# Kernel tuning notes

Hardware: AMD Instinct MI355X
Metric: run time of the kernel (lower is better)

## Reference

```python
import math
import jax
import jax.numpy as jnp
import numpy as np
from jax import lax

NH = 256       # n_hidden
KS = 5         # kernel_size
STRIDE = 2
DEPTH_VARIANT = True
B = 64
T = 4096


def _conv1d(x, w, b, stride):
    # x: [B, Cin, L], w: [Cout, Cin, K], torch-style symmetric padding (K-1)//2
    p = (w.shape[2] - 1) // 2
    y = lax.conv_general_dilated(x, w, window_strides=(stride,),
                                 padding=[(p, p)],
                                 dimension_numbers=('NCH', 'OIH', 'NCH'))
    return y + b[None, :, None]


def _seq_mask(x, N):
    m = jnp.arange(x.shape[2])[None, :] < N[:, None]
    return x * m[:, None, :].astype(x.dtype)


def setup_inputs() -> dict:
    key = jax.random.key(0)
    k1, k2, k3, k4, k5, k6 = jax.random.split(key, 6)
    h = jax.random.normal(k1, (B, NH, T), dtype=jnp.float32)
    N = jax.random.randint(k2, (B,), 1, T + 1, dtype=jnp.int32)
    cin1 = NH + (1 if DEPTH_VARIANT else 0)
    s1 = 1.0 / math.sqrt(cin1 * KS)
    s2 = 1.0 / math.sqrt(NH * KS)
    w1 = jax.random.uniform(k3, (2 * NH, cin1, KS), jnp.float32, -s1, s1)
    b1 = jax.random.uniform(k4, (2 * NH,), jnp.float32, -s1, s1)
    w2 = jax.random.uniform(k5, (NH, NH, KS), jnp.float32, -s2, s2)
    b2 = jax.random.uniform(k6, (NH,), jnp.float32, -s2, s2)
    return {"h": h, "N": N, "w1": w1, "b1": b1, "w2": w2, "b2": b2}


def reference(h, N, w1, b1, w2, b2):
    # Faithful to torch Reduce.forward (eval mode, dropout=0).
    # Instead of dynamically pruning finished rows, run all rows for the full
    # (statically known) number of reductions and capture h[:, :, 0] at the
    # depth where each row's N first drops to <= 1. The original output order
    # (grouped by finishing depth, original order within a group) is recovered
    # by a stable argsort on finish depth.
    nh = NH
    batch = h.shape[0]
    captured = jnp.zeros((batch, nh), h.dtype)
    finish_depth = jnp.zeros((batch,), jnp.int32)
    done = jnp.zeros((batch,), bool)
    depth = 0
    while True:
        if DEPTH_VARIANT:
            d = jnp.full((batch, 1, h.shape[2]), math.log1p(depth), h.dtype)
            hh = jnp.concatenate([h, d], axis=1)
        else:
            hh = h
        hh = _seq_mask(hh, N)
        lr = _conv1d(hh, w1, b1, STRIDE)
        N = (N - 1) // STRIDE + 1  # floor((N-1)/stride) + 1
        l = lr[:, :nh]
        r = jax.nn.relu(lr[:, nh:])
        r = _seq_mask(r, N)
        r = _conv1d(r, w2, b2, 1)
        h = jax.nn.relu(l + r)
        newly = (~done) & (N <= 1)
        captured = jnp.where(newly[:, None], h[:, :, 0], captured)
        finish_depth = jnp.where(newly, depth, finish_depth)
        done = done | newly
        depth += 1
        if h.shape[2] <= 1:  # static time length; N <= L so all rows are done
            break
    order = jnp.argsort(finish_depth, stable=True)
    return captured[order]
```

## Files before the change

kernel.cpp:

```cpp
#include <hip/hip_runtime.h>
#include <cmath>
#include <cstdint>


typedef __attribute__((ext_vector_type(8))) __bf16 bf16x8;
typedef __attribute__((ext_vector_type(4))) float f32x4;

union U16B { uint4 u; bf16x8 b; };
__device__ __forceinline__ bf16x8 as_bf16x8(uint4 u) { U16B x; x.u = u; return x.b; }

__device__ __forceinline__ unsigned short bf_hi_bits(float x) {
    union { __bf16 b; unsigned short s; } u; u.b = (__bf16)x; return u.s;
}
__device__ __forceinline__ float bf_hi_f(float x) { return (float)(__bf16)x; }

#define MFMA(a, b, c) __builtin_amdgcn_mfma_f32_16x16x32_bf16(a, b, c, 0, 0, 0)

__global__ void setup_kernel(const int* __restrict__ N0, int* __restrict__ rankfd) {
    __shared__ int fd_s[64];
    int b = threadIdx.x;
    int n = N0[b];
    int d = 0;
    while ((1 << (d + 1)) < n) ++d;
    fd_s[b] = d;
    __syncthreads();
    int myfd = fd_s[b];
    int r = 0;
    for (int i = 0; i < 64; ++i) {
        int f = fd_s[i];
        r += (f < myfd || (f == myfd && i < b)) ? 1 : 0;
    }
    rankfd[b] = r;
    rankfd[64 + b] = myfd;
}

__global__ void prepack_kernel(const float* __restrict__ w1, const float* __restrict__ w2,
                               unsigned short* __restrict__ Whi1, unsigned short* __restrict__ Wlo1,
                               unsigned short* __restrict__ Whi2, unsigned short* __restrict__ Wlo2,
                               float* __restrict__ wd1, float* __restrict__ wsum1) {
    const int T1 = 40 * 32 * 512;
    const int T2 = 40 * 16 * 512;
    int id = blockIdx.x * 256 + threadIdx.x;
    if (id < T1) {
        int chunk = id >> 14;
        int rem = id & 16383;
        int ot = rem >> 9;
        int rem2 = rem & 511;
        int l = rem2 >> 3, j = rem2 & 7;
        int k = chunk >> 3, cc = chunk & 7;
        int oc = ot * 16 + (l & 15);
        int c = cc * 32 + (l >> 4) * 8 + j;
        float wv = w1[oc * 1285 + c * 5 + k];
        Whi1[id] = bf_hi_bits(wv);
        Wlo1[id] = bf_hi_bits(wv - bf_hi_f(wv));
    } else if (id < T1 + T2) {
        int base = id - T1;
        int chunk = base >> 13;
        int rem = base & 8191;
        int ot = rem >> 9;
        int rem2 = rem & 511;
        int l = rem2 >> 3, j = rem2 & 7;
        int k = chunk >> 3, cc = chunk & 7;
        int oc = ot * 16 + (l & 15);
        int c = cc * 32 + (l >> 4) * 8 + j;
        float wv = w2[oc * 1280 + c * 5 + k];
        Whi2[base] = bf_hi_bits(wv);
        Wlo2[base] = bf_hi_bits(wv - bf_hi_f(wv));
    } else if (id < T1 + T2 + 512) {
        int oc = id - T1 - T2;
        float s = 0.f;
        for (int k = 0; k < 5; ++k) {
            float wv = w1[oc * 1285 + 1280 + k];
            wd1[oc * 5 + k] = wv;
            s += wv;
        }
        wsum1[oc] = s;
    }
}

__global__ __launch_bounds__(256, 4)
void transpose_kernel(const float* __restrict__ h, const int* __restrict__ N0,
                      char* __restrict__ H) {
    __shared__ unsigned short sm[2 * 64 * 140];
    const int tid = threadIdx.x;
    const int b = blockIdx.z;
    const int c0 = blockIdx.y * 64;
    const int t0 = blockIdx.x * 128;
    const int n0 = N0[b];
    const int lane32 = tid & 31;
    for (int it = 0; it < 8; ++it) {
        int cl = (tid >> 5) * 8 + it;
        const float* src = h + ((size_t)(b * 256 + c0 + cl)) * 4096 + t0 + lane32 * 4;
        float4 v = *(const float4*)src;
        int gt = t0 + lane32 * 4;
        float f[4] = {v.x, v.y, v.z, v.w};
        ushort4 hi, lo;
        unsigned short* hp = &hi.x;
        unsigned short* lp = &lo.x;
#pragma unroll
        for (int e = 0; e < 4; ++e) {
            float x = (gt + e < n0) ? f[e] : 0.f;
            float xh = bf_hi_f(x);
            hp[e] = bf_hi_bits(x);
            lp[e] = bf_hi_bits(x - xh);
        }
        *(ushort4*)(&sm[cl * 140 + lane32 * 4]) = hi;
        *(ushort4*)(&sm[8960 + cl * 140 + lane32 * 4]) = lo;
    }
    __syncthreads();
    const int sub = tid & 7;
    const int rowp = tid >> 3;
    for (int rep = 0; rep < 8; ++rep) {
        int idx = rowp + 32 * rep;
        int tl = idx >> 1;
        int plane = idx & 1;
        union { unsigned short s[8]; uint4 u; } pk;
#pragma unroll
        for (int j = 0; j < 8; ++j)
            pk.s[j] = sm[plane * 8960 + (sub * 8 + j) * 140 + tl];
        char* dst = H + ((size_t)(b * 4096) + t0 + tl) * 1024 + plane * 512 + c0 * 2 + sub * 16;
        *(uint4*)dst = pk.u;
    }
}

__global__ __launch_bounds__(256, 4)
void conv1_kernel(const char* __restrict__ Hin,
                  const unsigned short* __restrict__ Whi, const unsigned short* __restrict__ Wlo,
                  const float* __restrict__ b1, const float* __restrict__ wd1,
                  const float* __restrict__ wsum1, const int* __restrict__ N0,
                  float* __restrict__ Lout, char* __restrict__ Rout,
                  int T_in, int T_out, int depth, float logd) {
    __shared__ __align__(16) char smem[132 * 256];
    const int tid = threadIdx.x;
    const int w = tid >> 6, l = tid & 63;
    const int b = blockIdx.z;
    const int x_eff = (int)((blockIdx.x + 5u * (blockIdx.z >> 2)) & (gridDim.x - 1));
    const int t0 = x_eff * 64;
    const int n0 = N0[b];
    const int Nb = (n0 + (1 << depth) - 1) >> depth;
    const int Nn = (Nb + 1) >> 1;

    if (t0 >= Nn) {
        if (blockIdx.y == 1) {
            int row = t0 + (tid >> 2);
            if (row < T_out) {
                char* rp = Rout + ((size_t)(b * T_out) + row) * 1024 + (tid & 3) * 256;
                uint4 z = make_uint4(0, 0, 0, 0);
#pragma unroll
                for (int qq = 0; qq < 16; ++qq) *(uint4*)(rp + qq * 16) = z;
            }
        }
        return;
    }

    f32x4 acc[4][4];
#pragma unroll
    for (int i = 0; i < 4; ++i)
#pragma unroll
        for (int j = 0; j < 4; ++j) acc[i][j] = f32x4{0.f, 0.f, 0.f, 0.f};

    const int base_p = 2 * t0 - 2;
    const int otg_base = blockIdx.y * 16 + w * 4;

    const int sg_g8 = l & 7;
    const int sg_seg = (l >> 3) & 1;
    const int sg_rb0 = tid >> 4;

#pragma unroll 1
    for (int q0 = 0; q0 < 4; ++q0) {
        if (q0) __syncthreads();
        for (int rb = sg_rb0; rb < 132; rb += 16) {
            int p = base_p + rb;
            uint4 v = make_uint4(0, 0, 0, 0);
            if (p >= 0 && p < T_in)
                v = *(const uint4*)(Hin + ((size_t)(b * T_in) + p) * 1024 + sg_seg * 512 + q0 * 128 + sg_g8 * 16);
            int s = (rb >> 1) + (rb & 1) * 66;
            int phys = (sg_g8 ^ (s & 7)) | (sg_seg << 3);
            *(uint4*)(smem + s * 256 + phys * 16) = v;
        }
        __syncthreads();
#pragma unroll
        for (int k = 0; k < 5; ++k) {
#pragma unroll
            for (int ccl = 0; ccl < 2; ++ccl) {
                const int chunk = k * 8 + q0 * 2 + ccl;
                bf16x8 Bh[4], Bl[4];
#pragma unroll
                for (int tt = 0; tt < 4; ++tt) {
                    int s = tt * 16 + (l & 15) + (k >> 1) + (k & 1) * 66;
                    int gB = ccl * 4 + (l >> 4);
                    int ph = gB ^ (s & 7);
                    Bh[tt] = as_bf16x8(*(const uint4*)(smem + s * 256 + ph * 16));
                    Bl[tt] = as_bf16x8(*(const uint4*)(smem + s * 256 + (ph | 8) * 16));
                }
#pragma unroll
                for (int ot = 0; ot < 4; ++ot) {
                    size_t aoff = ((size_t)(chunk * 32 + otg_base + ot)) * 512 + l * 8;
                    bf16x8 Ah = as_bf16x8(*(const uint4*)(Whi + aoff));
                    bf16x8 Al = as_bf16x8(*(const uint4*)(Wlo + aoff));
#pragma unroll
                    for (int tt = 0; tt < 4; ++tt) {
                        acc[ot][tt] = MFMA(Ah, Bh[tt], acc[ot][tt]);
                        acc[ot][tt] = MFMA(Ah, Bl[tt], acc[ot][tt]);
                        acc[ot][tt] = MFMA(Al, Bh[tt], acc[ot][tt]);
                    }
                }
            }
        }
    }

    const int q = l >> 4;
    const int n = l & 15;
    const bool is_r = (blockIdx.y == 1);
#pragma unroll
    for (int ot = 0; ot < 4; ++ot) {
        const int ocg0 = (otg_base + ot) * 16 + q * 4;
        float4 bias = *(const float4*)(b1 + ocg0);
        float4 ws4 = *(const float4*)(wsum1 + ocg0);
#pragma unroll
        for (int tt = 0; tt < 4; ++tt) {
            int t = t0 + tt * 16 + n;
            if (t >= T_out) continue;
            float v0 = acc[ot][tt].x, v1 = acc[ot][tt].y, v2 = acc[ot][tt].z, v3 = acc[ot][tt].w;
            if (depth > 0) {
                if (t >= 1 && 2 * t + 2 < Nb) {
                    v0 += logd * ws4.x; v1 += logd * ws4.y;
                    v2 += logd * ws4.z; v3 += logd * ws4.w;
                } else {
                    float ind[5];
#pragma unroll
                    for (int k = 0; k < 5; ++k) {
                        int p = 2 * t + k - 2;
                        ind[k] = (p >= 0 && p < Nb) ? logd : 0.f;
                    }
                    float sv[4] = {0.f, 0.f, 0.f, 0.f};
#pragma unroll
                    for (int j = 0; j < 4; ++j)
#pragma unroll
                        for (int k = 0; k < 5; ++k) sv[j] += ind[k] * wd1[(ocg0 + j) * 5 + k];
                    v0 += sv[0]; v1 += sv[1]; v2 += sv[2]; v3 += sv[3];
                }
            }
            v0 += bias.x; v1 += bias.y; v2 += bias.z; v3 += bias.w;
            if (!is_r) {
                float4 o; o.x = v0; o.y = v1; o.z = v2; o.w = v3;
                *(float4*)(Lout + ((size_t)(b * T_out) + t) * 256 + ocg0) = o;
            } else {
                bool live = (t < Nn);
                float r0v = live ? fmaxf(v0, 0.f) : 0.f;
                float r1v = live ? fmaxf(v1, 0.f) : 0.f;
                float r2v = live ? fmaxf(v2, 0.f) : 0.f;
                float r3v = live ? fmaxf(v3, 0.f) : 0.f;
                int ocr = ocg0 - 256;
                char* rrow = Rout + ((size_t)(b * T_out) + t) * 1024;
                ushort4 H, L2;
                H.x = bf_hi_bits(r0v); L2.x = bf_hi_bits(r0v - bf_hi_f(r0v));
                H.y = bf_hi_bits(r1v); L2.y = bf_hi_bits(r1v - bf_hi_f(r1v));
                H.z = bf_hi_bits(r2v); L2.z = bf_hi_bits(r2v - bf_hi_f(r2v));
                H.w = bf_hi_bits(r3v); L2.w = bf_hi_bits(r3v - bf_hi_f(r3v));
                *(ushort4*)(rrow + ocr * 2) = H;
                *(ushort4*)(rrow + 512 + ocr * 2) = L2;
            }
        }
    }
}

__global__ __launch_bounds__(256, 4)
void conv2_kernel(const char* __restrict__ Rin,
                  const unsigned short* __restrict__ Whi, const unsigned short* __restrict__ Wlo,
                  const float* __restrict__ b2, const int* __restrict__ N0,
                  const int* __restrict__ rankfd, float* __restrict__ LH,
                  float* __restrict__ out, int T, int depth) {
    __shared__ __align__(16) char smem[68 * 512];
    const int tid = threadIdx.x;
    const int w = tid >> 6, l = tid & 63;
    const int b = blockIdx.z;
    const int x_eff = (int)((blockIdx.x + 5u * (blockIdx.z >> 2)) & (gridDim.x - 1));
    const int t0 = x_eff * 64;
    const int n0 = N0[b];
    const int Nn = (n0 + (1 << (depth + 1)) - 1) >> (depth + 1);

    if (t0 >= Nn) {
        int row = t0 + (tid >> 2);
        if (row < T) {
            char* hp = (char*)LH + ((size_t)(b * T) + row) * 1024 + (tid & 3) * 256;
            uint4 z = make_uint4(0, 0, 0, 0);
#pragma unroll
            for (int qq = 0; qq < 16; ++qq) *(uint4*)(hp + qq * 16) = z;
        }
        return;
    }

    f32x4 acc[4][4];
#pragma unroll
    for (int i = 0; i < 4; ++i)
#pragma unroll
        for (int j = 0; j < 4; ++j) acc[i][j] = f32x4{0.f, 0.f, 0.f, 0.f};

    const int sg_g16 = l & 15;
    const int sg_seg = (l >> 4) & 1;
    const int sg_rb0 = w * 2 + (l >> 5);

#pragma unroll 1
    for (int hf = 0; hf < 2; ++hf) {
        if (hf) __syncthreads();
        for (int rb = sg_rb0; rb < 68; rb += 8) {
            int p = t0 - 2 + rb;
            uint4 v = make_uint4(0, 0, 0, 0);
            if (p >= 0 && p < T)
                v = *(const uint4*)(Rin + ((size_t)(b * T) + p) * 1024 + sg_seg * 512 + hf * 256 + sg_g16 * 16);
            int phys = (sg_g16 ^ (rb & 7)) | (sg_seg << 4);
            *(uint4*)(smem + rb * 512 + phys * 16) = v;
        }
        __syncthreads();
#pragma unroll
        for (int k = 0; k < 5; ++k) {
#pragma unroll
            for (int cc = 0; cc < 4; ++cc) {
                const int chunk = k * 8 + hf * 4 + cc;
                bf16x8 Bh[4], Bl[4];
#pragma unroll
                for (int tt = 0; tt < 4; ++tt) {
                    int s = tt * 16 + (l & 15) + k;
                    int gq = cc * 4 + (l >> 4);
                    int ph = gq ^ (s & 7);
                    Bh[tt] = as_bf16x8(*(const uint4*)(smem + s * 512 + ph * 16));
                    Bl[tt] = as_bf16x8(*(const uint4*)(smem + s * 512 + (ph | 16) * 16));
                }
#pragma unroll
                for (int ot = 0; ot < 4; ++ot) {
                    size_t aoff = ((size_t)(chunk * 16 + w * 4 + ot)) * 512 + l * 8;
                    bf16x8 Ah = as_bf16x8(*(const uint4*)(Whi + aoff));
                    bf16x8 Al = as_bf16x8(*(const uint4*)(Wlo + aoff));
#pragma unroll
                    for (int tt = 0; tt < 4; ++tt) {
                        acc[ot][tt] = MFMA(Ah, Bh[tt], acc[ot][tt]);
                        acc[ot][tt] = MFMA(Ah, Bl[tt], acc[ot][tt]);
                        acc[ot][tt] = MFMA(Al, Bh[tt], acc[ot][tt]);
                    }
                }
            }
        }
    }

    const int q = l >> 4;
    const int n = l & 15;
    const int rk = rankfd[b];
    const int fd = rankfd[64 + b];
#pragma unroll
    for (int ot = 0; ot < 4; ++ot) {
        const int ocg0 = (w * 4 + ot) * 16 + q * 4;
        float4 bias = *(const float4*)(b2 + ocg0);
#pragma unroll
        for (int tt = 0; tt < 4; ++tt) {
            int t = t0 + tt * 16 + n;
            float v0 = 0.f, v1 = 0.f, v2 = 0.f, v3 = 0.f;
            if (t < T && t < Nn) {
                float4 l4 = *(const float4*)(LH + ((size_t)(b * T) + t) * 256 + ocg0);
                v0 = fmaxf(acc[ot][tt].x + l4.x + bias.x, 0.f);
                v1 = fmaxf(acc[ot][tt].y + l4.y + bias.y, 0.f);
                v2 = fmaxf(acc[ot][tt].z + l4.z + bias.z, 0.f);
                v3 = fmaxf(acc[ot][tt].w + l4.w + bias.w, 0.f);
                if (t == 0 && depth == fd) {
                    float4 o; o.x = v0; o.y = v1; o.z = v2; o.w = v3;
                    *(float4*)(out + rk * 256 + ocg0) = o;
                }
            }
            acc[ot][tt] = f32x4{v0, v1, v2, v3};
        }
    }
    __syncthreads();
#pragma unroll
    for (int ot = 0; ot < 4; ++ot) {
        const int ocg0 = (w * 4 + ot) * 16 + q * 4;
#pragma unroll
        for (int tt = 0; tt < 4; ++tt) {
            int t = t0 + tt * 16 + n;
            if (t >= T) continue;
            char* hrow = (char*)LH + ((size_t)(b * T) + t) * 1024;
            float v0 = acc[ot][tt].x, v1 = acc[ot][tt].y, v2 = acc[ot][tt].z, v3 = acc[ot][tt].w;
            ushort4 H, L2;
            H.x = bf_hi_bits(v0); L2.x = bf_hi_bits(v0 - bf_hi_f(v0));
            H.y = bf_hi_bits(v1); L2.y = bf_hi_bits(v1 - bf_hi_f(v1));
            H.z = bf_hi_bits(v2); L2.z = bf_hi_bits(v2 - bf_hi_f(v2));
            H.w = bf_hi_bits(v3); L2.w = bf_hi_bits(v3 - bf_hi_f(v3));
            *(ushort4*)(hrow + ocg0 * 2) = H;
            *(ushort4*)(hrow + 512 + ocg0 * 2) = L2;
        }
    }
}

extern "C" void kernel_launch(void* const* d_in, const int* in_sizes, int n_in,
                              void* d_out, int out_size, void* d_ws, size_t ws_size,
                              hipStream_t stream) {
    const float* h  = (const float*)d_in[0];
    const int*   N0 = (const int*)d_in[1];
    const float* w1 = (const float*)d_in[2];
    const float* b1 = (const float*)d_in[3];
    const float* w2 = (const float*)d_in[4];
    const float* b2 = (const float*)d_in[5];
    float* out = (float*)d_out;

    char* ws = (char*)d_ws;
    size_t off = 0;
    auto alloc = [&](size_t bytes) -> void* {
        void* p = ws + off;
        off = (off + bytes + 255) & ~(size_t)255;
        return p;
    };
    int* rankfd            = (int*)alloc(512);
    float* wd1             = (float*)alloc(512 * 5 * 4);
    float* wsum1           = (float*)alloc(512 * 4);
    unsigned short* Whi1   = (unsigned short*)alloc((size_t)655360 * 2);
    unsigned short* Wlo1   = (unsigned short*)alloc((size_t)655360 * 2);
    unsigned short* Whi2   = (unsigned short*)alloc((size_t)327680 * 2);
    unsigned short* Wlo2   = (unsigned short*)alloc((size_t)327680 * 2);
    float* P1              = (float*)alloc((size_t)64 * 2048 * 1024);
    char*  H4096           = (char*)alloc((size_t)64 * 4096 * 1024);
    float* P0              = (float*)H4096;
    char*  R               = (char*)alloc((size_t)64 * 2048 * 1024);
    (void)ws_size;

    setup_kernel<<<1, 64, 0, stream>>>(N0, rankfd);
    {
        int total = 655360 + 327680 + 512;
        prepack_kernel<<<(total + 255) / 256, 256, 0, stream>>>(w1, w2, Whi1, Wlo1, Whi2, Wlo2, wd1, wsum1);
    }
    transpose_kernel<<<dim3(32, 4, 64), 256, 0, stream>>>(h, N0, H4096);

    int T_in = 4096;
    for (int d = 0; d < 12; ++d) {
        int To = T_in >> 1;
        float* LH = (d & 1) ? P0 : P1;
        const char* Hin = (d == 0) ? (const char*)H4096 : (const char*)((d & 1) ? P1 : P0);
        float logd = log1pf((float)d);
        dim3 g1((To + 63) / 64, 2, 64);
        conv1_kernel<<<g1, 256, 0, stream>>>(Hin, Whi1, Wlo1, b1, wd1, wsum1, N0,
                                             LH, R, T_in, To, d, logd);
        dim3 g2((To + 63) / 64, 1, 64);
        conv2_kernel<<<g2, 256, 0, stream>>>(R, Whi2, Wlo2, b2, N0, rankfd, LH, out, To, d);
        T_in = To;
    }
}
```

Baseline: 2.621 ms.

## Fuse input transpose and bf16 split into first-depth conv1 tile load

Removes the separate transpose kernel that converted the fp32 [B,C,T] input into a time-major hi/lo bf16 buffer. At depth 0 the conv1 kernel now reads fp32 input rows directly, masks by N, splits into hi/lo bf16 and scatters into the swizzled shared-memory tile. This avoids a full write and re-read of a 256MB intermediate, but the depth-0 load is a strided scalar scatter into LDS with 2-byte stores, and each input element is reread by both output-channel blocks.

```diff
diff --git a/kernel.cpp b/kernel.cpp
--- a/kernel.cpp
+++ b/kernel.cpp
@@ -79,52 +79,7 @@
 }
 
 __global__ __launch_bounds__(256, 4)
-void transpose_kernel(const float* __restrict__ h, const int* __restrict__ N0,
-                      char* __restrict__ H) {
-    __shared__ unsigned short sm[2 * 64 * 140];
-    const int tid = threadIdx.x;
-    const int b = blockIdx.z;
-    const int c0 = blockIdx.y * 64;
-    const int t0 = blockIdx.x * 128;
-    const int n0 = N0[b];
-    const int lane32 = tid & 31;
-    for (int it = 0; it < 8; ++it) {
-        int cl = (tid >> 5) * 8 + it;
-        const float* src = h + ((size_t)(b * 256 + c0 + cl)) * 4096 + t0 + lane32 * 4;
-        float4 v = *(const float4*)src;
-        int gt = t0 + lane32 * 4;
-        float f[4] = {v.x, v.y, v.z, v.w};
-        ushort4 hi, lo;
-        unsigned short* hp = &hi.x;
-        unsigned short* lp = &lo.x;
-#pragma unroll
-        for (int e = 0; e < 4; ++e) {
-            float x = (gt + e < n0) ? f[e] : 0.f;
-            float xh = bf_hi_f(x);
-            hp[e] = bf_hi_bits(x);
-            lp[e] = bf_hi_bits(x - xh);
-        }
-        *(ushort4*)(&sm[cl * 140 + lane32 * 4]) = hi;
-        *(ushort4*)(&sm[8960 + cl * 140 + lane32 * 4]) = lo;
-    }
-    __syncthreads();
-    const int sub = tid & 7;
-    const int rowp = tid >> 3;
-    for (int rep = 0; rep < 8; ++rep) {
-        int idx = rowp + 32 * rep;
-        int tl = idx >> 1;
-        int plane = idx & 1;
-        union { unsigned short s[8]; uint4 u; } pk;
-#pragma unroll
-        for (int j = 0; j < 8; ++j)
-            pk.s[j] = sm[plane * 8960 + (sub * 8 + j) * 140 + tl];
-        char* dst = H + ((size_t)(b * 4096) + t0 + tl) * 1024 + plane * 512 + c0 * 2 + sub * 16;
-        *(uint4*)dst = pk.u;
-    }
-}
-
-__global__ __launch_bounds__(256, 4)
-void conv1_kernel(const char* __restrict__ Hin,
+void conv1_kernel(const float* __restrict__ h0, const char* __restrict__ Hin,
                   const unsigned short* __restrict__ Whi, const unsigned short* __restrict__ Wlo,
                   const float* __restrict__ b1, const float* __restrict__ wd1,
                   const float* __restrict__ wsum1, const int* __restrict__ N0,
@@ -166,17 +121,52 @@
     const int sg_seg = (l >> 3) & 1;
     const int sg_rb0 = tid >> 4;
 
+    const int f_oct = tid >> 5;
+    const int f_g = tid & 31;
+    const int f_cl = f_g >> 2;
+    const int f_i0 = f_g & 3;
+    const int al = base_p & ~3;
+
 #pragma unroll 1
     for (int q0 = 0; q0 < 4; ++q0) {
         if (q0) __syncthreads();
-        for (int rb = sg_rb0; rb < 132; rb += 16) {
-            int p = base_p + rb;
-            uint4 v = make_uint4(0, 0, 0, 0);
-            if (p >= 0 && p < T_in)
-                v = *(const uint4*)(Hin + ((size_t)(b * T_in) + p) * 1024 + sg_seg * 512 + q0 * 128 + sg_g8 * 16);
-            int s = (rb >> 1) + (rb & 1) * 66;
-            int phys = (sg_g8 ^ (s & 7)) | (sg_seg << 3);
-            *(uint4*)(smem + s * 256 + phys * 16) = v;
+        if (depth == 0) {
+            const float* hch = h0 + ((size_t)(b * 256 + q0 * 64 + f_oct * 8 + f_cl)) * 4096;
+#pragma unroll 1
+            for (int m = 0; m < 9; ++m) {
+                int p4 = al + 4 * (f_i0 + 4 * m);
+                float fe0 = 0.f, fe1 = 0.f, fe2 = 0.f, fe3 = 0.f;
+                if (p4 >= 0 && p4 < n0) {
+                    float4 v = *(const float4*)(hch + p4);
+                    fe0 = v.x;
+                    fe1 = (p4 + 1 < n0) ? v.y : 0.f;
+                    fe2 = (p4 + 2 < n0) ? v.z : 0.f;
+                    fe3 = (p4 + 3 < n0) ? v.w : 0.f;
+                }
+                float fe[4] = {fe0, fe1, fe2, fe3};
+#pragma unroll
+                for (int e = 0; e < 4; ++e) {
+                    int rb = p4 + e - base_p;
+                    if (rb >= 0 && rb < 132) {
+                        int s = (rb >> 1) + (rb & 1) * 66;
+                        int byte_hi = s * 256 + ((f_oct ^ (s & 7)) * 16) + f_cl * 2;
+                        float x = fe[e];
+                        float xh = bf_hi_f(x);
+                        *(unsigned short*)(smem + byte_hi) = bf_hi_bits(x);
+                        *(unsigned short*)(smem + byte_hi + 128) = bf_hi_bits(x - xh);
+                    }
+                }
+            }
+        } else {
+            for (int rb = sg_rb0; rb < 132; rb += 16) {
+                int p = base_p + rb;
+                uint4 v = make_uint4(0, 0, 0, 0);
+                if (p >= 0 && p < T_in)
+                    v = *(const uint4*)(Hin + ((size_t)(b * T_in) + p) * 1024 + sg_seg * 512 + q0 * 128 + sg_g8 * 16);
+                int s = (rb >> 1) + (rb & 1) * 66;
+                int phys = (sg_g8 ^ (s & 7)) | (sg_seg << 3);
+                *(uint4*)(smem + s * 256 + phys * 16) = v;
+            }
         }
         __syncthreads();
 #pragma unroll
@@ -416,8 +406,8 @@
     unsigned short* Whi2   = (unsigned short*)alloc((size_t)327680 * 2);
     unsigned short* Wlo2   = (unsigned short*)alloc((size_t)327680 * 2);
     float* P1              = (float*)alloc((size_t)64 * 2048 * 1024);
-    char*  H4096           = (char*)alloc((size_t)64 * 4096 * 1024);
-    float* P0              = (float*)H4096;
+    char*  P0c             = (char*)alloc((size_t)64 * 4096 * 1024);
+    float* P0              = (float*)P0c;
     char*  R               = (char*)alloc((size_t)64 * 2048 * 1024);
     (void)ws_size;
 
@@ -426,16 +416,15 @@
         int total = 655360 + 327680 + 512;
         prepack_kernel<<<(total + 255) / 256, 256, 0, stream>>>(w1, w2, Whi1, Wlo1, Whi2, Wlo2, wd1, wsum1);
     }
-    transpose_kernel<<<dim3(32, 4, 64), 256, 0, stream>>>(h, N0, H4096);
 
     int T_in = 4096;
     for (int d = 0; d < 12; ++d) {
         int To = T_in >> 1;
         float* LH = (d & 1) ? P0 : P1;
-        const char* Hin = (d == 0) ? (const char*)H4096 : (const char*)((d & 1) ? P1 : P0);
+        const char* Hin = (const char*)((d & 1) ? P1 : P0);
         float logd = log1pf((float)d);
         dim3 g1((To + 63) / 64, 2, 64);
-        conv1_kernel<<<g1, 256, 0, stream>>>(Hin, Whi1, Wlo1, b1, wd1, wsum1, N0,
+        conv1_kernel<<<g1, 256, 0, stream>>>(h, Hin, Whi1, Wlo1, b1, wd1, wsum1, N0,
                                              LH, R, T_in, To, d, logd);
         dim3 g2((To + 63) / 64, 1, 64);
         conv2_kernel<<<g2, 256, 0, stream>>>(R, Whi2, Wlo2, b2, N0, rankfd, LH, out, To, d);
```

New measurement: 2.560 ms. -2.3%, faster.
